# Kernel optimization log

Measured on AMD Instinct MI355X. Metric: run time of the kernel, lower is better.

The kernel has to match this reference:

```python
import jax, jax.numpy as jnp
import numpy as np

D, H, K, L, F, G, M, OUT = 1280, 16, 80, 4, 5120, 48, 2, 2048
HALF = K // 2  # rotary half dim = 40


def _token_coords(grid_thw, merge_size, N):
    tpi = grid_thw[:, 0] * grid_thw[:, 1] * grid_thw[:, 2]
    cu = jnp.concatenate([jnp.zeros(1, jnp.int32), jnp.cumsum(tpi).astype(jnp.int32)])
    tok = jnp.arange(N, dtype=jnp.int32)
    img_id = jnp.searchsorted(cu[1:], tok, side='right')
    local = tok - cu[img_id]
    h = grid_thw[img_id, 1]
    w = grid_thw[img_id, 2]
    spatial = local % (h * w)
    msq = merge_size * merge_size
    mw = w // merge_size
    group, intra = spatial // msq, spatial % msq
    row = (group // mw) * merge_size + intra // merge_size
    col = (group % mw) * merge_size + intra % merge_size
    return row, col, h, w, cu


def _layernorm(x, s, b, eps=1e-6):
    mu = jnp.mean(x, -1, keepdims=True)
    var = jnp.mean(jnp.square(x - mu), -1, keepdims=True)
    return (x - mu) * jax.lax.rsqrt(var + eps) * s + b


def _rotate_half(x):
    x1, x2 = x[..., :HALF], x[..., HALF:]
    return jnp.concatenate([-x2, x1], axis=-1)


def setup_inputs() -> dict:
    key = jax.random.key(0)
    ks = jax.random.split(key, 16)
    s = 0.02
    inp = {
        'pixels': jax.random.normal(ks[0], (2048, 1536), jnp.float32),
        'grid_thw': jnp.array([[1, 16, 32]] * 4, jnp.int32),
        'pos_embed': jax.random.normal(ks[1], (G * G, D), jnp.float32) * s,
        'patch_w': jax.random.normal(ks[2], (1536, D), jnp.float32) * s,
        'patch_b': jnp.zeros((D,), jnp.float32),
        'ln1_s': jnp.ones((L, D), jnp.float32), 'ln1_b': jnp.zeros((L, D), jnp.float32),
        'qkv_w': jax.random.normal(ks[3], (L, D, 3 * D), jnp.float32) * s,
        'qkv_b': jnp.zeros((L, 3 * D), jnp.float32),
        'proj_w': jax.random.normal(ks[4], (L, D, D), jnp.float32) * s,
        'proj_b': jnp.zeros((L, D), jnp.float32),
        'ln2_s': jnp.ones((L, D), jnp.float32), 'ln2_b': jnp.zeros((L, D), jnp.float32),
        'fc1_w': jax.random.normal(ks[5], (L, D, F), jnp.float32) * s,
        'fc1_b': jnp.zeros((L, F), jnp.float32),
        'fc2_w': jax.random.normal(ks[6], (L, F, D), jnp.float32) * s,
        'fc2_b': jnp.zeros((L, D), jnp.float32),
        'm_norm_s': jnp.ones((D,), jnp.float32), 'm_norm_b': jnp.zeros((D,), jnp.float32),
        'm_fc1_w': jax.random.normal(ks[7], (D * M * M, D * M * M), jnp.float32) * s,
        'm_fc1_b': jnp.zeros((D * M * M,), jnp.float32),
        'm_fc2_w': jax.random.normal(ks[8], (D * M * M, OUT), jnp.float32) * s,
        'm_fc2_b': jnp.zeros((OUT,), jnp.float32),
    }
    return inp


def _forward(pixels, grid_thw, pos_embed, patch_w, patch_b, ln1_s, ln1_b, qkv_w, qkv_b,
             proj_w, proj_b, ln2_s, ln2_b, fc1_w, fc1_b, fc2_w, fc2_b,
             m_norm_s, m_norm_b, m_fc1_w, m_fc1_b, m_fc2_w, m_fc2_b):
    N = pixels.shape[0]
    row, col, h, w, cu = _token_coords(grid_thw, M, N)

    # patch embed: conv with stride==kernel over flattened patches == linear
    x = pixels @ patch_w + patch_b  # [N, D]

    # bilinear position-embedding interpolation onto each image's (h, w) grid
    rf = jnp.where(h > 1, row.astype(jnp.float32) * (G - 1) / jnp.maximum(h - 1, 1), 0.0)
    cf = jnp.where(w > 1, col.astype(jnp.float32) * (G - 1) / jnp.maximum(w - 1, 1), 0.0)
    r0 = jnp.floor(rf).astype(jnp.int32); r1 = jnp.minimum(r0 + 1, G - 1)
    c0 = jnp.floor(cf).astype(jnp.int32); c1 = jnp.minimum(c0 + 1, G - 1)
    wr = (rf - r0)[:, None]; wc = (cf - c0)[:, None]
    pe = (pos_embed[r0 * G + c0] * (1 - wr) * (1 - wc)
          + pos_embed[r0 * G + c1] * (1 - wr) * wc
          + pos_embed[r1 * G + c0] * wr * (1 - wc)
          + pos_embed[r1 * G + c1] * wr * wc)
    x = x + pe

    # 2-D rotary embeddings
    inv_freq = 1.0 / (10000.0 ** (jnp.arange(0, HALF, 2, dtype=jnp.float32) / HALF))
    freqs = jnp.concatenate([row[:, None].astype(jnp.float32) * inv_freq,
                             col[:, None].astype(jnp.float32) * inv_freq], axis=-1)  # [N, HALF]
    emb = jnp.concatenate([freqs, freqs], axis=-1)  # [N, K]
    cos, sin = jnp.cos(emb)[:, None, :], jnp.sin(emb)[:, None, :]  # [N,1,K]

    # block-diagonal segment mask via cu_seqlens (N is a multiple of 128; no pad)
    tok = jnp.arange(N)
    seg = jnp.searchsorted(cu[1:], tok, side='right')
    k_start = cu[jnp.minimum(seg, cu.shape[0] - 2)]
    k_end = cu[jnp.minimum(seg + 1, cu.shape[0] - 1)]
    mask = (tok[None, :] >= k_start[:, None]) & (tok[None, :] < k_end[:, None])  # [N,N]
    scale = K ** -0.5

    for l in range(L):
        hdn = _layernorm(x, ln1_s[l], ln1_b[l])
        qkv = (hdn @ qkv_w[l] + qkv_b[l]).reshape(N, 3, H, K)
        q, k, v = qkv[:, 0], qkv[:, 1], qkv[:, 2]
        q = q * cos + _rotate_half(q) * sin
        k = k * cos + _rotate_half(k) * sin
        scores = jnp.einsum('nhk,mhk->hnm', q, k) * scale
        scores = jnp.where(mask[None], scores, jnp.finfo(scores.dtype).min)
        attn = jax.nn.softmax(scores, axis=-1)
        o = jnp.einsum('hnm,mhk->nhk', attn, v).reshape(N, D)
        x = x + o @ proj_w[l] + proj_b[l]

        hdn = _layernorm(x, ln2_s[l], ln2_b[l])
        ff = jax.nn.gelu(hdn @ fc1_w[l] + fc1_b[l], approximate=True)
        x = x + ff @ fc2_w[l] + fc2_b[l]

    # patch merger
    normed = _layernorm(x, m_norm_s, m_norm_b).reshape(N // (M * M), D * M * M)
    ff = jax.nn.gelu(normed @ m_fc1_w + m_fc1_b, approximate=True)
    return ff @ m_fc2_w + m_fc2_b  # [N/4, OUT]


def reference(pixels, grid_thw, pos_embed, patch_w, patch_b, ln1_s, ln1_b, qkv_w, qkv_b,
              proj_w, proj_b, ln2_s, ln2_b, fc1_w, fc1_b, fc2_w, fc2_b,
              m_norm_s, m_norm_b, m_fc1_w, m_fc1_b, m_fc2_w, m_fc2_b):
    return _forward(pixels, grid_thw, pos_embed, patch_w, patch_b, ln1_s, ln1_b, qkv_w, qkv_b,
                    proj_w, proj_b, ln2_s, ln2_b, fc1_w, fc1_b, fc2_w, fc2_b,
                    m_norm_s, m_norm_b, m_fc1_w, m_fc1_b, m_fc2_w, m_fc2_b)
```

## Files before the change

kernel.cpp:

```cpp
#include <hip/hip_runtime.h>
#include <math.h>

#define DMODEL 1280
#define NHEADS 16
#define FDIM   5120
#define GPOS   48
#define SEG    512

typedef __attribute__((ext_vector_type(8))) short bf16x8;
typedef __attribute__((ext_vector_type(4))) float f32x4;
typedef unsigned short u16;

__device__ __forceinline__ u16 f2bf(float f) {
  unsigned int u = __float_as_uint(f);
  u = (u + 0x7FFFu + ((u >> 16) & 1u)) >> 16;
  return (u16)u;
}
__device__ __forceinline__ float bf2f(u16 u) {
  return __uint_as_float((unsigned int)u << 16);
}
__device__ __forceinline__ float gelu_tanh(float x) {
  float u = 0.7978845608028654f * (x + 0.044715f * x * x * x);
  float t = __expf(2.f * u);
  float th = 1.f - 2.f / (t + 1.f);
  return 0.5f * x * (1.f + th);
}

typedef const __attribute__((address_space(1))) unsigned int* gas_t;
typedef __attribute__((address_space(3))) unsigned int* las_t;
__device__ __forceinline__ void async16(const void* g, void* l) {
  __builtin_amdgcn_global_load_lds((gas_t)g, (las_t)l, 16, 0, 0);
}

#define STG256(mat, PW, ldx, h, kk, pp)                          \
  do {                                                           \
    const u16* g_ = (PW) + (long long)(h) * 128 * (ldx) + (kk);  \
    async16(g_, &L[pp][mat][h][(w * 2 + 0) * 512]);              \
    async16(g_ + 32, &L[pp][mat][h][(w * 2 + 1) * 512]);         \
  } while (0)

#define MM256(ii, ff)                                                          \
  acc[ii][ff] = __builtin_amdgcn_mfma_f32_16x16x32_bf16(aR[(ii) & 3][0],       \
                    bR[ff][0], acc[ii][ff], 0, 0, 0);                          \
  acc[ii][ff] = __builtin_amdgcn_mfma_f32_16x16x32_bf16(aR[(ii) & 3][1],       \
                    bR[ff][1], acc[ii][ff], 0, 0, 0);

#define BAR256() asm volatile("s_barrier" ::: "memory")
#define LGKM0() asm volatile("s_waitcnt lgkmcnt(0)" ::: "memory")

template <int EPI>
__global__ __launch_bounds__(512, 2) void gemm256(
    const u16* __restrict__ A, const u16* __restrict__ B,
    const float* __restrict__ bias, void* __restrict__ Cv,
    int Kd, int lda, int ldb, int ldc, int nsplit, long long pstride) {
  __shared__ __align__(16) u16 L[2][2][2][8192];
  const int sp = blockIdx.z;
  const int Ks = Kd / nsplit;
  const int NT = Ks >> 6;
  const u16* Ab = A + (long long)sp * Ks;
  const u16* Bb = B + (long long)sp * Ks;
  const int m0 = blockIdx.x * 256, n0 = blockIdx.y * 256;
  const int t = threadIdx.x, ln = t & 63, w = t >> 6;
  const int wr = w >> 2, wc = w & 3;
  const int m16 = ln & 15, q = ln >> 4;
  const int r16 = ln >> 2;
  const int csw = (ln & 3) ^ (ln >> 4);
  const int rbase = m16 * 32 + ((q ^ (m16 >> 2)) & 3) * 8;

  const u16* Aw = Ab + (long long)(m0 + w * 16 + r16) * lda + csw * 8;
  const u16* Bw = Bb + (long long)(n0 + w * 16 + r16) * ldb + csw * 8;

  f32x4 acc[8][4];
#pragma unroll
  for (int i = 0; i < 8; i++)
#pragma unroll
    for (int j = 0; j < 4; j++)
#pragma unroll
      for (int r = 0; r < 4; r++) acc[i][j][r] = 0.f;

  STG256(0, Aw, lda, 0, 0, 0);
  STG256(0, Aw, lda, 1, 0, 0);
  STG256(1, Bw, ldb, 0, 0, 0);
  STG256(1, Bw, ldb, 1, 0, 0);
  if (NT > 1) {
    STG256(1, Bw, ldb, 0, 64, 1);
    STG256(1, Bw, ldb, 1, 64, 1);
    asm volatile("s_waitcnt vmcnt(4)" ::: "memory");
  } else {
    asm volatile("s_waitcnt vmcnt(0)" ::: "memory");
  }
  BAR256();

  const int wb = (wc & 1) * 4;
  for (int tt = 0; tt < NT; ++tt) {
    const int p = tt & 1;
    const u16* Abuf = &L[p][0][wr][0];
    const u16* Bbuf = &L[p][1][wc >> 1][0];
    bf16x8 aR[4][2], bR[4][2];

#pragma unroll
    for (int i = 0; i < 4; ++i) {
      aR[i][0] = *(const bf16x8*)(Abuf + (i * 2 + 0) * 512 + rbase);
      aR[i][1] = *(const bf16x8*)(Abuf + (i * 2 + 1) * 512 + rbase);
    }
#pragma unroll
    for (int fc = 0; fc < 2; ++fc) {
      bR[fc][0] = *(const bf16x8*)(Bbuf + ((wb + fc) * 2 + 0) * 512 + rbase);
      bR[fc][1] = *(const bf16x8*)(Bbuf + ((wb + fc) * 2 + 1) * 512 + rbase);
    }
    if (tt + 1 < NT) STG256(0, Aw, lda, 0, (tt + 1) * 64, (tt + 1) & 1);
    BAR256();
    LGKM0();
    __builtin_amdgcn_s_setprio(1);
#pragma unroll
    for (int i = 0; i < 4; ++i) { MM256(i, 0); MM256(i, 1); }
    __builtin_amdgcn_s_setprio(0);
    BAR256();

#pragma unroll
    for (int fc = 2; fc < 4; ++fc) {
      bR[fc][0] = *(const bf16x8*)(Bbuf + ((wb + fc) * 2 + 0) * 512 + rbase);
      bR[fc][1] = *(const bf16x8*)(Bbuf + ((wb + fc) * 2 + 1) * 512 + rbase);
    }
    if (tt + 1 < NT) STG256(0, Aw, lda, 1, (tt + 1) * 64, (tt + 1) & 1);
    BAR256();
    LGKM0();
    __builtin_amdgcn_s_setprio(1);
#pragma unroll
    for (int i = 0; i < 4; ++i) { MM256(i, 2); MM256(i, 3); }
    __builtin_amdgcn_s_setprio(0);
    BAR256();

#pragma unroll
    for (int i = 0; i < 4; ++i) {
      aR[i][0] = *(const bf16x8*)(Abuf + ((4 + i) * 2 + 0) * 512 + rbase);
      aR[i][1] = *(const bf16x8*)(Abuf + ((4 + i) * 2 + 1) * 512 + rbase);
    }
    if (tt + 2 < NT) STG256(1, Bw, ldb, 0, (tt + 2) * 64, p);
    BAR256();
    LGKM0();
    __builtin_amdgcn_s_setprio(1);
#pragma unroll
    for (int i = 0; i < 4; ++i) { MM256(4 + i, 2); MM256(4 + i, 3); }
    __builtin_amdgcn_s_setprio(0);
    BAR256();

    if (tt + 2 < NT) STG256(1, Bw, ldb, 1, (tt + 2) * 64, p);
    BAR256();
    LGKM0();
    __builtin_amdgcn_s_setprio(1);
#pragma unroll
    for (int i = 0; i < 4; ++i) { MM256(4 + i, 0); MM256(4 + i, 1); }
    __builtin_amdgcn_s_setprio(0);
    if (tt + 1 < NT) {
      if (tt + 2 < NT) asm volatile("s_waitcnt vmcnt(4)" ::: "memory");
      else             asm volatile("s_waitcnt vmcnt(0)" ::: "memory");
    }
    BAR256();
  }

#pragma unroll
  for (int fr = 0; fr < 8; fr++) {
#pragma unroll
    for (int r = 0; r < 4; r++) {
      int row = m0 + wr * 128 + fr * 16 + q * 4 + r;
      if (EPI == 0) {
        u16* Cp = (u16*)Cv + (long long)sp * pstride + (long long)row * ldc;
#pragma unroll
        for (int fc = 0; fc < 4; fc++)
          Cp[n0 + wc * 64 + fc * 16 + m16] = f2bf(acc[fr][fc][r]);
      } else if (EPI == 1) {
        u16* Cb = (u16*)Cv + (long long)row * ldc;
#pragma unroll
        for (int fc = 0; fc < 4; fc++) {
          int col = n0 + wc * 64 + fc * 16 + m16;
          Cb[col] = f2bf(acc[fr][fc][r] + bias[col]);
        }
      } else {
        u16* Cb = (u16*)Cv + (long long)row * ldc;
#pragma unroll
        for (int fc = 0; fc < 4; fc++) {
          int col = n0 + wc * 64 + fc * 16 + m16;
          Cb[col] = f2bf(gelu_tanh(acc[fr][fc][r] + bias[col]));
        }
      }
    }
  }
}

__global__ __launch_bounds__(256) void fattn_k(
    const u16* __restrict__ qr, const u16* __restrict__ kr,
    const u16* __restrict__ vpT, u16* __restrict__ o, int N, float iscale) {
  __shared__ __align__(16) u16 Ks[2][24][512];
  __shared__ __align__(16) u16 Vs[2][20][512];
  __shared__ __align__(16) u16 Ps[4][32 * 128];
  const int nseg = N >> 9;
  const int hb = blockIdx.y;
  const int h = hb / nseg, seg = hb - h * nseg;
  const int t = threadIdx.x, ln = t & 63, w = t >> 6;
  const int m16 = ln & 15, qh = ln >> 4;
  const int r4 = ln >> 2, gsw = (ln & 3) ^ (ln >> 4);
  const int rbase = m16 * 32 + ((qh ^ (m16 >> 2)) & 3) * 8;
  const long long hN = (long long)h * N;
  const int segbase = seg * SEG;
  const int q0 = segbase + blockIdx.x * 128 + w * 32;

  bf16x8 qf[2][3];
#pragma unroll
  for (int mi = 0; mi < 2; mi++)
#pragma unroll
    for (int ks = 0; ks < 3; ks++)
      qf[mi][ks] = *(const bf16x8*)&qr[(hN + q0 + mi * 16 + m16) * 96 + ks * 32 + qh * 8];

  f32x4 ao[2][5];
#pragma unroll
  for (int mi = 0; mi < 2; mi++)
#pragma unroll
    for (int df = 0; df < 5; df++)
#pragma unroll
      for (int r = 0; r < 4; r++) ao[mi][df][r] = 0.f;
  float m_[2][4], l_[2][4];
#pragma unroll
  for (int mi = 0; mi < 2; mi++)
#pragma unroll
    for (int r = 0; r < 4; r++) { m_[mi][r] = -1e30f; l_[mi][r] = 0.f; }

  auto stage = [&](int c, int pb) {
#pragma unroll
    for (int i = 0; i < 6; i++) {
      int sK = w * 6 + i, f = sK / 3, kg = sK - f * 3;
      async16(&kr[(hN + segbase + c * 128 + f * 16 + r4) * 96 + kg * 32 + gsw * 8],
              &Ks[pb][sK][0]);
    }
#pragma unroll
    for (int i = 0; i < 5; i++) {
      int sV = w * 5 + i, df = sV >> 2, kvg = sV & 3;
      async16(&vpT[((long long)hb * 128 + df * 16 + r4) * SEG + c * 128 + kvg * 32 + gsw * 8],
              &Vs[pb][sV][0]);
    }
  };

  stage(0, 0);
  u16* Pmy = &Ps[w][0];
  for (int c = 0; c < 4; c++) {
    const int pb = c & 1;
    __syncthreads();
    if (c < 3) stage(c + 1, pb ^ 1);

    f32x4 s[2][8];
#pragma unroll
    for (int mi = 0; mi < 2; mi++)
#pragma unroll
      for (int f = 0; f < 8; f++)
#pragma unroll
        for (int r = 0; r < 4; r++) s[mi][f][r] = 0.f;
#pragma unroll
    for (int ks = 0; ks < 3; ks++) {
#pragma unroll
      for (int f = 0; f < 8; f++) {
        bf16x8 kf = *(const bf16x8*)&Ks[pb][f * 3 + ks][rbase];
#pragma unroll
        for (int mi = 0; mi < 2; mi++)
          s[mi][f] = __builtin_amdgcn_mfma_f32_16x16x32_bf16(qf[mi][ks], kf, s[mi][f], 0, 0, 0);
      }
    }

#pragma unroll
    for (int mi = 0; mi < 2; mi++) {
#pragma unroll
      for (int r = 0; r < 4; r++) {
        float mx = s[mi][0][r];
#pragma unroll
        for (int f = 1; f < 8; f++) mx = fmaxf(mx, s[mi][f][r]);
        mx *= iscale;
#pragma unroll
        for (int o2 = 1; o2 <= 8; o2 <<= 1) mx = fmaxf(mx, __shfl_xor(mx, o2));
        float mn = fmaxf(m_[mi][r], mx);
        float corr = __expf(m_[mi][r] - mn);
        m_[mi][r] = mn;
        float rs = 0.f;
#pragma unroll
        for (int f = 0; f < 8; f++) {
          float p = __expf(s[mi][f][r] * iscale - mn);
          s[mi][f][r] = p;
          rs += p;
        }
#pragma unroll
        for (int o2 = 1; o2 <= 8; o2 <<= 1) rs += __shfl_xor(rs, o2);
        l_[mi][r] = l_[mi][r] * corr + rs;
#pragma unroll
        for (int df = 0; df < 5; df++) ao[mi][df][r] *= corr;
      }
    }

#pragma unroll
    for (int mi = 0; mi < 2; mi++) {
#pragma unroll
      for (int r = 0; r < 4; r++) {
        int qq = mi * 16 + qh * 4 + r;
        int base = qq * 128 + (m16 & 7);
        int ql = qq & 7;
#pragma unroll
        for (int f = 0; f < 8; f++) {
          int gr = (f * 2 + (m16 >> 3)) ^ ql;
          Pmy[base + gr * 8] = f2bf(s[mi][f][r]);
        }
      }
    }

#pragma unroll
    for (int ks = 0; ks < 4; ks++) {
      bf16x8 pf[2];
#pragma unroll
      for (int mi = 0; mi < 2; mi++)
        pf[mi] = *(const bf16x8*)&Pmy[(mi * 16 + m16) * 128 +
                                      (((ks * 4 + qh) ^ (m16 & 7)) << 3)];
#pragma unroll
      for (int df = 0; df < 5; df++) {
        bf16x8 vf = *(const bf16x8*)&Vs[pb][df * 4 + ks][rbase];
#pragma unroll
        for (int mi = 0; mi < 2; mi++)
          ao[mi][df] = __builtin_amdgcn_mfma_f32_16x16x32_bf16(pf[mi], vf, ao[mi][df], 0, 0, 0);
      }
    }
  }

#pragma unroll
  for (int mi = 0; mi < 2; mi++) {
#pragma unroll
    for (int r = 0; r < 4; r++) {
      float rl = 1.f / l_[mi][r];
      long long rowb = (long long)(q0 + mi * 16 + qh * 4 + r) * DMODEL + h * 80;
#pragma unroll
      for (int df = 0; df < 5; df++)
        o[rowb + df * 16 + m16] = f2bf(ao[mi][df][r] * rl);
    }
  }
}

template <int S, int RES, int GELU, int OUTBF>
__global__ void reduce_k(const u16* __restrict__ Pp, long long mn, int Nn,
                         const float* __restrict__ bias,
                         const float* __restrict__ res, void* __restrict__ out) {
  long long i = ((long long)blockIdx.x * 256 + threadIdx.x) * 4;
  if (i >= mn) return;
  float vx = 0.f, vy = 0.f, vz = 0.f, vw = 0.f;
#pragma unroll
  for (int s = 0; s < S; s++) {
    ushort4 u4 = *(const ushort4*)(Pp + (long long)s * mn + i);
    vx += bf2f(u4.x); vy += bf2f(u4.y); vz += bf2f(u4.z); vw += bf2f(u4.w);
  }
  int col = (int)(i % Nn);
  vx += bias[col]; vy += bias[col + 1]; vz += bias[col + 2]; vw += bias[col + 3];
  if (GELU) {
    vx = gelu_tanh(vx); vy = gelu_tanh(vy);
    vz = gelu_tanh(vz); vw = gelu_tanh(vw);
  }
  if (RES) {
    float4 r4 = *(const float4*)(res + i);
    vx += r4.x; vy += r4.y; vz += r4.z; vw += r4.w;
  }
  if (OUTBF) {
    ushort4 o; o.x = f2bf(vx); o.y = f2bf(vy); o.z = f2bf(vz); o.w = f2bf(vw);
    *(ushort4*)((u16*)out + i) = o;
  } else {
    float4 o; o.x = vx; o.y = vy; o.z = vz; o.w = vw;
    *(float4*)((float*)out + i) = o;
  }
}

__global__ void wconv_k(const float* __restrict__ in, u16* __restrict__ out,
                        int K, int N) {
  __shared__ float tl[32][33];
  int n0 = blockIdx.x * 32, k0 = blockIdx.y * 32;
  int t = threadIdx.x;
  int r = t >> 5, c = t & 31;
#pragma unroll
  for (int i = 0; i < 4; i++)
    tl[r + 8 * i][c] = in[(long long)(k0 + r + 8 * i) * N + n0 + c];
  __syncthreads();
  int n = t >> 4, kp = (t & 15) * 2;
#pragma unroll
  for (int i = 0; i < 2; i++) {
    ushort2 o;
    o.x = f2bf(tl[kp][n + 16 * i]);
    o.y = f2bf(tl[kp + 1][n + 16 * i]);
    *(ushort2*)&out[(long long)(n0 + n + 16 * i) * K + k0 + kp] = o;
  }
}

__global__ void conv_k(const float* __restrict__ in, u16* __restrict__ out,
                       long long n) {
  long long i = ((long long)blockIdx.x * 256 + threadIdx.x) * 4;
  if (i >= n) return;
  float4 v = *(const float4*)(in + i);
  ushort4 o; o.x = f2bf(v.x); o.y = f2bf(v.y); o.z = f2bf(v.z); o.w = f2bf(v.w);
  *(ushort4*)&out[i] = o;
}

union U16x8 { uint4 v; u16 s[8]; };
__global__ void vtr_k(const u16* __restrict__ in, u16* __restrict__ out) {
  __shared__ u16 tl[64][65];
  int b = blockIdx.z;
  int m0 = blockIdx.x * 64;
  int d0 = blockIdx.y * 64;
  const u16* ib = in + (long long)b * SEG * 128;
  u16* ob = out + (long long)b * 128 * SEG;
  int t = threadIdx.x;
  int r = t >> 3, c8 = (t & 7) * 8;
#pragma unroll
  for (int i = 0; i < 2; i++) {
    U16x8 ld;
    ld.v = *(const uint4*)&ib[(long long)(m0 + r + 32 * i) * 128 + d0 + c8];
#pragma unroll
    for (int j = 0; j < 8; j++) tl[r + 32 * i][c8 + j] = ld.s[j];
  }
  __syncthreads();
  int d = t >> 3, m8 = (t & 7) * 8;
#pragma unroll
  for (int i = 0; i < 2; i++) {
    int dd = d + 32 * i;
    U16x8 st;
#pragma unroll
    for (int j = 0; j < 8; j++) st.s[j] = tl[m8 + j][dd];
    *(uint4*)&ob[(long long)(d0 + dd) * SEG + m0 + m8] = st.v;
  }
}

__global__ void coords_k(const int* __restrict__ g, int nimg,
                         int* __restrict__ rw, int* __restrict__ cl,
                         int* __restrict__ hh, int* __restrict__ ww, int N) {
  int t = blockIdx.x * 256 + threadIdx.x;
  if (t >= N) return;
  int c = 0, local = 0, H = 1, W = 1;
  for (int i = 0; i < nimg; i++) {
    int tpi = g[i * 3] * g[i * 3 + 1] * g[i * 3 + 2];
    if (t >= c && t < c + tpi) { local = t - c; H = g[i * 3 + 1]; W = g[i * 3 + 2]; }
    c += tpi;
  }
  int hw = H * W;
  int sp = local % hw;
  int mw = W >> 1;
  int gr = sp >> 2, intra = sp & 3;
  rw[t] = (gr / mw) * 2 + (intra >> 1);
  cl[t] = (gr % mw) * 2 + (intra & 1);
  hh[t] = H; ww[t] = W;
}

__global__ void peadd_k(float* __restrict__ x, const float* __restrict__ pe,
                        const int* __restrict__ rw, const int* __restrict__ cl,
                        const int* __restrict__ hh, const int* __restrict__ ww) {
  int n = blockIdx.x;
  int d = threadIdx.x * 4;
  int H = hh[n], W = ww[n];
  float rf = (H > 1) ? (float)rw[n] * (float)(GPOS - 1) / (float)(H - 1) : 0.f;
  float cf = (W > 1) ? (float)cl[n] * (float)(GPOS - 1) / (float)(W - 1) : 0.f;
  int r0 = (int)floorf(rf), c0 = (int)floorf(cf);
  int r1 = min(r0 + 1, GPOS - 1), c1 = min(c0 + 1, GPOS - 1);
  float wr = rf - (float)r0, wc = cf - (float)c0;
  float w00 = (1.f - wr) * (1.f - wc), w01 = (1.f - wr) * wc;
  float w10 = wr * (1.f - wc), w11 = wr * wc;
  float4 v00 = *(const float4*)(pe + (long long)(r0 * GPOS + c0) * DMODEL + d);
  float4 v01 = *(const float4*)(pe + (long long)(r0 * GPOS + c1) * DMODEL + d);
  float4 v10 = *(const float4*)(pe + (long long)(r1 * GPOS + c0) * DMODEL + d);
  float4 v11 = *(const float4*)(pe + (long long)(r1 * GPOS + c1) * DMODEL + d);
  float4 xv = *(float4*)(x + (long long)n * DMODEL + d);
  xv.x += w00 * v00.x + w01 * v01.x + w10 * v10.x + w11 * v11.x;
  xv.y += w00 * v00.y + w01 * v01.y + w10 * v10.y + w11 * v11.y;
  xv.z += w00 * v00.z + w01 * v01.z + w10 * v10.z + w11 * v11.z;
  xv.w += w00 * v00.w + w01 * v01.w + w10 * v10.w + w11 * v11.w;
  *(float4*)(x + (long long)n * DMODEL + d) = xv;
}

__global__ void ln_k(const float* __restrict__ X, u16* __restrict__ Y,
                     const float* __restrict__ s, const float* __restrict__ b) {
  int row = blockIdx.x;
  int d = threadIdx.x * 4;
  const float* x = X + (long long)row * DMODEL;
  float4 v = *(const float4*)(x + d);
  float sum = v.x + v.y + v.z + v.w;
#pragma unroll
  for (int o = 32; o; o >>= 1) sum += __shfl_xor(sum, o);
  __shared__ float red[8];
  int wv = threadIdx.x >> 6, lnn = threadIdx.x & 63;
  if (lnn == 0) red[wv] = sum;
  __syncthreads();
  float mu = 0.f;
  for (int i = 0; i < 5; i++) mu += red[i];
  mu *= (1.f / DMODEL);
  float dx = v.x - mu, dy = v.y - mu, dz = v.z - mu, dw = v.w - mu;
  float s2 = dx * dx + dy * dy + dz * dz + dw * dw;
#pragma unroll
  for (int o = 32; o; o >>= 1) s2 += __shfl_xor(s2, o);
  __syncthreads();
  if (lnn == 0) red[wv] = s2;
  __syncthreads();
  float var = 0.f;
  for (int i = 0; i < 5; i++) var += red[i];
  var *= (1.f / DMODEL);
  float rs = rsqrtf(var + 1e-6f);
  ushort4 o4;
  o4.x = f2bf(dx * rs * s[d] + b[d]);
  o4.y = f2bf(dy * rs * s[d + 1] + b[d + 1]);
  o4.z = f2bf(dz * rs * s[d + 2] + b[d + 2]);
  o4.w = f2bf(dw * rs * s[d + 3] + b[d + 3]);
  *(ushort4*)(Y + (long long)row * DMODEL + d) = o4;
}

__global__ void rope_k(const u16* __restrict__ qkv, const int* __restrict__ rw,
                       const int* __restrict__ cl, u16* __restrict__ qr,
                       u16* __restrict__ kr, u16* __restrict__ vp, int N) {
  int n = blockIdx.x, h = blockIdx.y, t = threadIdx.x;
  const u16* src = qkv + (long long)n * (3 * DMODEL) + h * 80;
  long long ob96 = ((long long)h * N + n) * 96;
  long long ob128 = ((long long)h * N + n) * 128;
  if (t < 40) {
    float pos = (t < 20) ? (float)rw[n] : (float)cl[n];
    float infr = exp2f(-13.287712379549449f * (float)(t % 20) * 0.05f);
    float f = pos * infr;
    float cs = cosf(f), sn = sinf(f);
    float q0 = bf2f(src[t]), q1 = bf2f(src[t + 40]);
    qr[ob96 + t] = f2bf(q0 * cs - q1 * sn);
    qr[ob96 + t + 40] = f2bf(q1 * cs + q0 * sn);
    float k0 = bf2f(src[DMODEL + t]), k1 = bf2f(src[DMODEL + t + 40]);
    kr[ob96 + t] = f2bf(k0 * cs - k1 * sn);
    kr[ob96 + t + 40] = f2bf(k1 * cs + k0 * sn);
    vp[ob128 + t] = src[2 * DMODEL + t];
    vp[ob128 + t + 40] = src[2 * DMODEL + t + 40];
  } else {
    int u = t - 40;
    if (u < 16) { qr[ob96 + 80 + u] = 0; kr[ob96 + 80 + u] = 0; }
    vp[ob128 + 80 + u] = 0;
    vp[ob128 + 104 + u] = 0;
  }
}

static void gemm_big(hipStream_t st, int epi, const u16* A, const u16* B,
                     const float* bias, void* C, int M, int Nn, int Kd,
                     int lda, int ldb, int ldc, int nsplit) {
  dim3 g(M / 256, Nn / 256, nsplit), blk(512);
  long long ps = (long long)M * Nn;
  switch (epi) {
    case 0: gemm256<0><<<g, blk, 0, st>>>(A, B, bias, C, Kd, lda, ldb, ldc, nsplit, ps); break;
    case 1: gemm256<1><<<g, blk, 0, st>>>(A, B, bias, C, Kd, lda, ldb, ldc, nsplit, ps); break;
    default: gemm256<3><<<g, blk, 0, st>>>(A, B, bias, C, Kd, lda, ldb, ldc, nsplit, ps); break;
  }
}

extern "C" void kernel_launch(void* const* d_in, const int* in_sizes, int n_in,
                              void* d_out, int out_size, void* d_ws, size_t ws_size,
                              hipStream_t stream) {
  const float* pixels = (const float*)d_in[0];
  const int* grid_thw = (const int*)d_in[1];
  const float* pos_embed = (const float*)d_in[2];
  const float* patch_w = (const float*)d_in[3];
  const float* patch_b = (const float*)d_in[4];
  const float* ln1_s = (const float*)d_in[5];
  const float* ln1_b = (const float*)d_in[6];
  const float* qkv_w = (const float*)d_in[7];
  const float* qkv_b = (const float*)d_in[8];
  const float* proj_w = (const float*)d_in[9];
  const float* proj_b = (const float*)d_in[10];
  const float* ln2_s = (const float*)d_in[11];
  const float* ln2_b = (const float*)d_in[12];
  const float* fc1_w = (const float*)d_in[13];
  const float* fc1_b = (const float*)d_in[14];
  const float* fc2_w = (const float*)d_in[15];
  const float* fc2_b = (const float*)d_in[16];
  const float* mns = (const float*)d_in[17];
  const float* mnb = (const float*)d_in[18];
  const float* mf1w = (const float*)d_in[19];
  const float* mf1b = (const float*)d_in[20];
  const float* mf2w = (const float*)d_in[21];
  const float* mf2b = (const float*)d_in[22];
  float* out = (float*)d_out;

  const int N = in_sizes[0] / 1536;
  const int nimg = in_sizes[1] / 3;
  const int nseg = N / SEG;
  const int nb = NHEADS * nseg;

  char* w = (char*)d_ws;
  size_t off = 0;
  auto alloc = [&](size_t bytes) -> void* {
    void* p = w + off;
    off += (bytes + 255) & ~(size_t)255;
    return p;
  };
  int* rw = (int*)alloc((size_t)N * 4);
  int* cl = (int*)alloc((size_t)N * 4);
  int* hh = (int*)alloc((size_t)N * 4);
  int* ww = (int*)alloc((size_t)N * 4);
  float* x = (float*)alloc((size_t)N * DMODEL * 4);
  u16* h = (u16*)alloc((size_t)N * DMODEL * 2);
  u16* pixbf = (u16*)alloc((size_t)N * 1536 * 2);
  u16* patchT = (u16*)alloc((size_t)DMODEL * 1536 * 2);
  u16* qkvT = (u16*)alloc((size_t)3 * DMODEL * DMODEL * 2);
  u16* projT = (u16*)alloc((size_t)DMODEL * DMODEL * 2);
  u16* fc1T = (u16*)alloc((size_t)FDIM * DMODEL * 2);
  u16* fc2T = (u16*)alloc((size_t)DMODEL * FDIM * 2);
  u16* qkvb = (u16*)alloc((size_t)N * 3 * DMODEL * 2);
  u16* qr = (u16*)alloc((size_t)NHEADS * N * 96 * 2);
  u16* kr = (u16*)alloc((size_t)NHEADS * N * 96 * 2);
  u16* vp = (u16*)alloc((size_t)NHEADS * N * 128 * 2);
  u16* vpT = (u16*)alloc((size_t)NHEADS * N * 128 * 2);
  u16* pad0 = (u16*)alloc((size_t)nb * 2 * SEG * 128 * 2);
  u16* o = (u16*)alloc((size_t)N * DMODEL * 2);
  float* bigA = (float*)alloc((size_t)nb * SEG * SEG * 4);
  float* bigB = (float*)alloc((size_t)nb * SEG * SEG * 2);
  (void)ws_size; (void)pad0;
  u16* mfc1T = qkvb;
  u16* mfc2T = pixbf;
  u16* ffb = (u16*)bigA;
  u16* mf = (u16*)bigA;
  u16* part = (u16*)bigB;

  const float iscale = 0.11180339887498949f;

  coords_k<<<dim3((N + 255) / 256), 256, 0, stream>>>(grid_thw, nimg, rw, cl, hh, ww, N);
  conv_k<<<dim3((int)(((long long)N * 1536 / 4 + 255) / 256)), 256, 0, stream>>>(
      pixels, pixbf, (long long)N * 1536);
  wconv_k<<<dim3(DMODEL / 32, 1536 / 32), 256, 0, stream>>>(patch_w, patchT, 1536, DMODEL);
  gemm_big(stream, 0, pixbf, patchT, nullptr, part, N, DMODEL, 1536, 1536, 1536,
           DMODEL, 4);
  reduce_k<4, 0, 0, 0><<<dim3((int)(((long long)N * DMODEL / 4 + 255) / 256)), 256, 0, stream>>>(
      part, (long long)N * DMODEL, DMODEL, patch_b, nullptr, x);
  peadd_k<<<dim3(N), 320, 0, stream>>>(x, pos_embed, rw, cl, hh, ww);

  for (int l = 0; l < 4; l++) {
    wconv_k<<<dim3(3 * DMODEL / 32, DMODEL / 32), 256, 0, stream>>>(
        qkv_w + (size_t)l * DMODEL * 3 * DMODEL, qkvT, DMODEL, 3 * DMODEL);
    wconv_k<<<dim3(DMODEL / 32, DMODEL / 32), 256, 0, stream>>>(
        proj_w + (size_t)l * DMODEL * DMODEL, projT, DMODEL, DMODEL);
    wconv_k<<<dim3(FDIM / 32, DMODEL / 32), 256, 0, stream>>>(
        fc1_w + (size_t)l * DMODEL * FDIM, fc1T, DMODEL, FDIM);
    wconv_k<<<dim3(DMODEL / 32, FDIM / 32), 256, 0, stream>>>(
        fc2_w + (size_t)l * FDIM * DMODEL, fc2T, FDIM, DMODEL);

    ln_k<<<dim3(N), 320, 0, stream>>>(x, h, ln1_s + l * DMODEL, ln1_b + l * DMODEL);
    gemm_big(stream, 1, h, qkvT, qkv_b + (size_t)l * 3 * DMODEL, qkvb, N,
             3 * DMODEL, DMODEL, DMODEL, DMODEL, 3 * DMODEL, 1);
    rope_k<<<dim3(N, NHEADS), 64, 0, stream>>>(qkvb, rw, cl, qr, kr, vp, N);
    vtr_k<<<dim3(8, 2, nb), 256, 0, stream>>>(vp, vpT);
    fattn_k<<<dim3(SEG / 128, nb), 256, 0, stream>>>(qr, kr, vpT, o, N, iscale);
    gemm_big(stream, 0, o, projT, nullptr, part, N, DMODEL, DMODEL, DMODEL,
             DMODEL, DMODEL, 4);
    reduce_k<4, 1, 0, 0><<<dim3((int)(((long long)N * DMODEL / 4 + 255) / 256)), 256, 0, stream>>>(
        part, (long long)N * DMODEL, DMODEL, proj_b + (size_t)l * DMODEL, x, x);
    ln_k<<<dim3(N), 320, 0, stream>>>(x, h, ln2_s + l * DMODEL, ln2_b + l * DMODEL);
    gemm_big(stream, 3, h, fc1T, fc1_b + (size_t)l * FDIM, ffb, N, FDIM, DMODEL,
             DMODEL, DMODEL, FDIM, 1);
    gemm_big(stream, 0, ffb, fc2T, nullptr, part, N, DMODEL, FDIM, FDIM, FDIM,
             DMODEL, 4);
    reduce_k<4, 1, 0, 0><<<dim3((int)(((long long)N * DMODEL / 4 + 255) / 256)), 256, 0, stream>>>(
        part, (long long)N * DMODEL, DMODEL, fc2_b + (size_t)l * DMODEL, x, x);
  }

  ln_k<<<dim3(N), 320, 0, stream>>>(x, h, mns, mnb);
  const int Mm = N / 4;
  wconv_k<<<dim3(FDIM / 32, FDIM / 32), 256, 0, stream>>>(mf1w, mfc1T, FDIM, FDIM);
  gemm_big(stream, 0, h, mfc1T, nullptr, part, Mm, FDIM, FDIM, FDIM, FDIM, FDIM, 4);
  reduce_k<4, 0, 1, 1><<<dim3((int)(((long long)Mm * FDIM / 4 + 255) / 256)), 256, 0, stream>>>(
      part, (long long)Mm * FDIM, FDIM, mf1b, nullptr, mf);
  wconv_k<<<dim3(2048 / 32, FDIM / 32), 256, 0, stream>>>(mf2w, mfc2T, FDIM, 2048);
  gemm_big(stream, 0, mf, mfc2T, nullptr, part, Mm, 2048, FDIM, FDIM, FDIM, 2048, 16);
  reduce_k<16, 0, 0, 0><<<dim3((int)(((long long)Mm * 2048 / 4 + 255) / 256)), 256, 0, stream>>>(
      part, (long long)Mm * 2048, 2048, mf2b, nullptr, out);
}
```

Baseline: 1.549 ms.

## Fuse split-K reduce with layernorm, reschedule GEMM prefetch and LDS swizzle

Adds a redln_k kernel that sums the split-K partials, adds bias and residual, writes x, and computes the next layernorm in one pass. This replaces the separate reduce_k and ln_k launches after the proj and fc2 GEMMs, and the following layer's ln1 (or the merger norm) is folded in. The GEMM main loop now prefetches whole A and B tiles two steps ahead with deeper vmcnt waits, and drops one LDS wait. The LDS swizzle pattern changes in both the GEMM and the attention kernel. The swizzle and pipeline edits risk bank conflicts or correctness problems if the read and write patterns are not kept consistent.

```diff
diff --git a/kernel.cpp b/kernel.cpp
--- a/kernel.cpp
+++ b/kernel.cpp
@@ -64,8 +64,8 @@
   const int wr = w >> 2, wc = w & 3;
   const int m16 = ln & 15, q = ln >> 4;
   const int r16 = ln >> 2;
-  const int csw = (ln & 3) ^ (ln >> 4);
-  const int rbase = m16 * 32 + ((q ^ (m16 >> 2)) & 3) * 8;
+  const int csw = (ln & 3) ^ ((ln >> 5) << 1);
+  const int rbase = m16 * 32 + (q ^ ((m16 >> 3) << 1)) * 8;
 
   const u16* Aw = Ab + (long long)(m0 + w * 16 + r16) * lda + csw * 8;
   const u16* Bw = Bb + (long long)(n0 + w * 16 + r16) * ldb + csw * 8;
@@ -78,14 +78,18 @@
 #pragma unroll
       for (int r = 0; r < 4; r++) acc[i][j][r] = 0.f;
 
-  STG256(0, Aw, lda, 0, 0, 0);
-  STG256(0, Aw, lda, 1, 0, 0);
-  STG256(1, Bw, ldb, 0, 0, 0);
-  STG256(1, Bw, ldb, 1, 0, 0);
+  auto stageT = [&](int tt, int pp) {
+    int kk = tt * 64;
+    STG256(0, Aw, lda, 0, kk, pp);
+    STG256(0, Aw, lda, 1, kk, pp);
+    STG256(1, Bw, ldb, 0, kk, pp);
+    STG256(1, Bw, ldb, 1, kk, pp);
+  };
+
+  stageT(0, 0);
   if (NT > 1) {
-    STG256(1, Bw, ldb, 0, 64, 1);
-    STG256(1, Bw, ldb, 1, 64, 1);
-    asm volatile("s_waitcnt vmcnt(4)" ::: "memory");
+    stageT(1, 1);
+    asm volatile("s_waitcnt vmcnt(8)" ::: "memory");
   } else {
     asm volatile("s_waitcnt vmcnt(0)" ::: "memory");
   }
@@ -108,7 +112,6 @@
       bR[fc][0] = *(const bf16x8*)(Bbuf + ((wb + fc) * 2 + 0) * 512 + rbase);
       bR[fc][1] = *(const bf16x8*)(Bbuf + ((wb + fc) * 2 + 1) * 512 + rbase);
     }
-    if (tt + 1 < NT) STG256(0, Aw, lda, 0, (tt + 1) * 64, (tt + 1) & 1);
     BAR256();
     LGKM0();
     __builtin_amdgcn_s_setprio(1);
@@ -122,7 +125,6 @@
       bR[fc][0] = *(const bf16x8*)(Bbuf + ((wb + fc) * 2 + 0) * 512 + rbase);
       bR[fc][1] = *(const bf16x8*)(Bbuf + ((wb + fc) * 2 + 1) * 512 + rbase);
     }
-    if (tt + 1 < NT) STG256(0, Aw, lda, 1, (tt + 1) * 64, (tt + 1) & 1);
     BAR256();
     LGKM0();
     __builtin_amdgcn_s_setprio(1);
@@ -136,7 +138,10 @@
       aR[i][0] = *(const bf16x8*)(Abuf + ((4 + i) * 2 + 0) * 512 + rbase);
       aR[i][1] = *(const bf16x8*)(Abuf + ((4 + i) * 2 + 1) * 512 + rbase);
     }
-    if (tt + 2 < NT) STG256(1, Bw, ldb, 0, (tt + 2) * 64, p);
+    if (tt + 2 < NT) {
+      STG256(1, Bw, ldb, 0, (tt + 2) * 64, p);
+      STG256(1, Bw, ldb, 1, (tt + 2) * 64, p);
+    }
     BAR256();
     LGKM0();
     __builtin_amdgcn_s_setprio(1);
@@ -145,17 +150,17 @@
     __builtin_amdgcn_s_setprio(0);
     BAR256();
 
-    if (tt + 2 < NT) STG256(1, Bw, ldb, 1, (tt + 2) * 64, p);
+    if (tt + 2 < NT) {
+      STG256(0, Aw, lda, 0, (tt + 2) * 64, p);
+      STG256(0, Aw, lda, 1, (tt + 2) * 64, p);
+    }
     BAR256();
-    LGKM0();
     __builtin_amdgcn_s_setprio(1);
 #pragma unroll
     for (int i = 0; i < 4; ++i) { MM256(4 + i, 0); MM256(4 + i, 1); }
     __builtin_amdgcn_s_setprio(0);
-    if (tt + 1 < NT) {
-      if (tt + 2 < NT) asm volatile("s_waitcnt vmcnt(4)" ::: "memory");
-      else             asm volatile("s_waitcnt vmcnt(0)" ::: "memory");
-    }
+    if (tt + 2 < NT)      asm volatile("s_waitcnt vmcnt(8)" ::: "memory");
+    else if (tt + 1 < NT) asm volatile("s_waitcnt vmcnt(0)" ::: "memory");
     BAR256();
   }
 
@@ -199,8 +204,8 @@
   const int h = hb / nseg, seg = hb - h * nseg;
   const int t = threadIdx.x, ln = t & 63, w = t >> 6;
   const int m16 = ln & 15, qh = ln >> 4;
-  const int r4 = ln >> 2, gsw = (ln & 3) ^ (ln >> 4);
-  const int rbase = m16 * 32 + ((qh ^ (m16 >> 2)) & 3) * 8;
+  const int r4 = ln >> 2, gsw = (ln & 3) ^ ((ln >> 5) << 1);
+  const int rbase = m16 * 32 + ((qh ^ ((m16 >> 3) << 1)) << 3);
   const long long hN = (long long)h * N;
   const int segbase = seg * SEG;
   const int q0 = segbase + blockIdx.x * 128 + w * 32;
@@ -367,6 +372,55 @@
     float4 o; o.x = vx; o.y = vy; o.z = vz; o.w = vw;
     *(float4*)((float*)out + i) = o;
   }
+}
+
+template <int S>
+__global__ void redln_k(const u16* __restrict__ Pp, long long mn,
+                        const float* __restrict__ bias,
+                        float* __restrict__ x,
+                        const float* __restrict__ s, const float* __restrict__ b,
+                        u16* __restrict__ h) {
+  int row = blockIdx.x;
+  int d = threadIdx.x * 4;
+  long long base = (long long)row * DMODEL + d;
+  float vx = 0.f, vy = 0.f, vz = 0.f, vw = 0.f;
+#pragma unroll
+  for (int si = 0; si < S; si++) {
+    ushort4 u4 = *(const ushort4*)(Pp + (long long)si * mn + base);
+    vx += bf2f(u4.x); vy += bf2f(u4.y); vz += bf2f(u4.z); vw += bf2f(u4.w);
+  }
+  vx += bias[d]; vy += bias[d + 1]; vz += bias[d + 2]; vw += bias[d + 3];
+  float4 r4 = *(const float4*)(x + base);
+  vx += r4.x; vy += r4.y; vz += r4.z; vw += r4.w;
+  float4 xv; xv.x = vx; xv.y = vy; xv.z = vz; xv.w = vw;
+  *(float4*)(x + base) = xv;
+  float sum = vx + vy + vz + vw;
+#pragma unroll
+  for (int o = 32; o; o >>= 1) sum += __shfl_xor(sum, o);
+  __shared__ float red[8];
+  int wv = threadIdx.x >> 6, lnn = threadIdx.x & 63;
+  if (lnn == 0) red[wv] = sum;
+  __syncthreads();
+  float mu = 0.f;
+  for (int i = 0; i < 5; i++) mu += red[i];
+  mu *= (1.f / DMODEL);
+  float dx = vx - mu, dy = vy - mu, dz = vz - mu, dw = vw - mu;
+  float s2 = dx * dx + dy * dy + dz * dz + dw * dw;
+#pragma unroll
+  for (int o = 32; o; o >>= 1) s2 += __shfl_xor(s2, o);
+  __syncthreads();
+  if (lnn == 0) red[wv] = s2;
+  __syncthreads();
+  float var = 0.f;
+  for (int i = 0; i < 5; i++) var += red[i];
+  var *= (1.f / DMODEL);
+  float rs = rsqrtf(var + 1e-6f);
+  ushort4 o4;
+  o4.x = f2bf(dx * rs * s[d] + b[d]);
+  o4.y = f2bf(dy * rs * s[d + 1] + b[d + 1]);
+  o4.z = f2bf(dz * rs * s[d + 2] + b[d + 2]);
+  o4.w = f2bf(dw * rs * s[d + 3] + b[d + 3]);
+  *(ushort4*)(h + base) = o4;
 }
 
 __global__ void wconv_k(const float* __restrict__ in, u16* __restrict__ out,
@@ -616,6 +670,7 @@
   u16* part = (u16*)bigB;
 
   const float iscale = 0.11180339887498949f;
+  const long long mnD = (long long)N * DMODEL;
 
   coords_k<<<dim3((N + 255) / 256), 256, 0, stream>>>(grid_thw, nimg, rw, cl, hh, ww, N);
   conv_k<<<dim3((int)(((long long)N * 1536 / 4 + 255) / 256)), 256, 0, stream>>>(
@@ -623,9 +678,10 @@
   wconv_k<<<dim3(DMODEL / 32, 1536 / 32), 256, 0, stream>>>(patch_w, patchT, 1536, DMODEL);
   gemm_big(stream, 0, pixbf, patchT, nullptr, part, N, DMODEL, 1536, 1536, 1536,
            DMODEL, 4);
-  reduce_k<4, 0, 0, 0><<<dim3((int)(((long long)N * DMODEL / 4 + 255) / 256)), 256, 0, stream>>>(
-      part, (long long)N * DMODEL, DMODEL, patch_b, nullptr, x);
+  reduce_k<4, 0, 0, 0><<<dim3((int)((mnD / 4 + 255) / 256)), 256, 0, stream>>>(
+      part, mnD, DMODEL, patch_b, nullptr, x);
   peadd_k<<<dim3(N), 320, 0, stream>>>(x, pos_embed, rw, cl, hh, ww);
+  ln_k<<<dim3(N), 320, 0, stream>>>(x, h, ln1_s, ln1_b);
 
   for (int l = 0; l < 4; l++) {
     wconv_k<<<dim3(3 * DMODEL / 32, DMODEL / 32), 256, 0, stream>>>(
@@ -637,7 +693,6 @@
     wconv_k<<<dim3(DMODEL / 32, FDIM / 32), 256, 0, stream>>>(
         fc2_w + (size_t)l * FDIM * DMODEL, fc2T, FDIM, DMODEL);
 
-    ln_k<<<dim3(N), 320, 0, stream>>>(x, h, ln1_s + l * DMODEL, ln1_b + l * DMODEL);
     gemm_big(stream, 1, h, qkvT, qkv_b + (size_t)l * 3 * DMODEL, qkvb, N,
              3 * DMODEL, DMODEL, DMODEL, DMODEL, 3 * DMODEL, 1);
     rope_k<<<dim3(N, NHEADS), 64, 0, stream>>>(qkvb, rw, cl, qr, kr, vp, N);
@@ -645,18 +700,19 @@
     fattn_k<<<dim3(SEG / 128, nb), 256, 0, stream>>>(qr, kr, vpT, o, N, iscale);
     gemm_big(stream, 0, o, projT, nullptr, part, N, DMODEL, DMODEL, DMODEL,
              DMODEL, DMODEL, 4);
-    reduce_k<4, 1, 0, 0><<<dim3((int)(((long long)N * DMODEL / 4 + 255) / 256)), 256, 0, stream>>>(
-        part, (long long)N * DMODEL, DMODEL, proj_b + (size_t)l * DMODEL, x, x);
-    ln_k<<<dim3(N), 320, 0, stream>>>(x, h, ln2_s + l * DMODEL, ln2_b + l * DMODEL);
+    redln_k<4><<<dim3(N), 320, 0, stream>>>(part, mnD, proj_b + (size_t)l * DMODEL,
+                                            x, ln2_s + (size_t)l * DMODEL,
+                                            ln2_b + (size_t)l * DMODEL, h);
     gemm_big(stream, 3, h, fc1T, fc1_b + (size_t)l * FDIM, ffb, N, FDIM, DMODEL,
              DMODEL, DMODEL, FDIM, 1);
     gemm_big(stream, 0, ffb, fc2T, nullptr, part, N, DMODEL, FDIM, FDIM, FDIM,
              DMODEL, 4);
-    reduce_k<4, 1, 0, 0><<<dim3((int)(((long long)N * DMODEL / 4 + 255) / 256)), 256, 0, stream>>>(
-        part, (long long)N * DMODEL, DMODEL, fc2_b + (size_t)l * DMODEL, x, x);
-  }
-
-  ln_k<<<dim3(N), 320, 0, stream>>>(x, h, mns, mnb);
+    const float* nsl = (l < 3) ? ln1_s + (size_t)(l + 1) * DMODEL : mns;
+    const float* nbl = (l < 3) ? ln1_b + (size_t)(l + 1) * DMODEL : mnb;
+    redln_k<4><<<dim3(N), 320, 0, stream>>>(part, mnD, fc2_b + (size_t)l * DMODEL,
+                                            x, nsl, nbl, h);
+  }
+
   const int Mm = N / 4;
   wconv_k<<<dim3(FDIM / 32, FDIM / 32), 256, 0, stream>>>(mf1w, mfc1T, FDIM, FDIM);
   gemm_big(stream, 0, h, mfc1T, nullptr, part, Mm, FDIM, FDIM, FDIM, FDIM, FDIM, 4);
```

New measurement: 1.506 ms. -2.8%, faster.
